# Kernel optimization log

Hardware: AMD Instinct MI355X
Metric: run time of the kernel (lower is better)

Reference implementation:

```python
import jax, jax.numpy as jnp
import numpy as np
from jax import lax

INPUT_DIM = 12
T = 2048
H = 512
L = 6
EPS = 1e-5


def setup_inputs() -> dict:
    key = jax.random.key(0)
    ks = jax.random.split(key, 12)
    s = 1.0 / np.sqrt(H)
    inp = {
        "x": jax.random.normal(ks[0], (32, INPUT_DIM), dtype=jnp.float32),
        "in_proj_w": jax.random.normal(ks[1], (H, INPUT_DIM), dtype=jnp.float32) * (1.0 / np.sqrt(INPUT_DIM)),
        "in_proj_b": jnp.zeros((H,), dtype=jnp.float32),
        "W_ih": jax.random.uniform(ks[2], (L, 4 * H, H), dtype=jnp.float32, minval=-s, maxval=s),
        "W_hh": jax.random.uniform(ks[3], (L, 4 * H, H), dtype=jnp.float32, minval=-s, maxval=s),
        "b_ih": jax.random.uniform(ks[4], (L, 4 * H), dtype=jnp.float32, minval=-s, maxval=s),
        "b_hh": jax.random.uniform(ks[5], (L, 4 * H), dtype=jnp.float32, minval=-s, maxval=s),
        "ln_scale": jnp.ones((L, H), dtype=jnp.float32),
        "ln_bias": jnp.zeros((L, H), dtype=jnp.float32),
        "out_w": jax.random.normal(ks[6], (1, H), dtype=jnp.float32) * s,
        "out_b": jnp.zeros((1,), dtype=jnp.float32),
    }
    return inp


def _lstm_layer(h_in, Wih, Whh, bih, bhh):
    # h_in: (B, T, H); PyTorch gate order: i, f, g, o
    B = h_in.shape[0]
    xg = jnp.einsum("bth,gh->btg", h_in, Wih) + bih  # (B, T, 4H) input gates precomputed
    xg_t = jnp.swapaxes(xg, 0, 1)  # (T, B, 4H)
    h0 = jnp.zeros((B, H), dtype=h_in.dtype)
    c0 = jnp.zeros((B, H), dtype=h_in.dtype)

    def step(carry, xt):
        h, c = carry
        gates = xt + h @ Whh.T + bhh
        i, f, g, o = jnp.split(gates, 4, axis=-1)
        i = jax.nn.sigmoid(i)
        f = jax.nn.sigmoid(f)
        g = jnp.tanh(g)
        o = jax.nn.sigmoid(o)
        c = f * c + i * g
        h = o * jnp.tanh(c)
        return (h, c), h

    _, hs = lax.scan(step, (h0, c0), xg_t)  # hs: (T, B, H)
    return jnp.swapaxes(hs, 0, 1)


def _layernorm(x, scale, bias):
    mu = jnp.mean(x, axis=-1, keepdims=True)
    var = jnp.mean(jnp.square(x - mu), axis=-1, keepdims=True)
    return (x - mu) * lax.rsqrt(var + EPS) * scale + bias


def reference(x, in_proj_w, in_proj_b, W_ih, W_hh, b_ih, b_hh, ln_scale, ln_bias, out_w, out_b):
    x_proj = x @ in_proj_w.T + in_proj_b  # (B, H)
    h = jnp.broadcast_to(x_proj[:, None, :], (x.shape[0], T, H))  # repeat along time
    for l in range(L):
        out = _lstm_layer(h, W_ih[l], W_hh[l], b_ih[l], b_hh[l])
        h = _layernorm(out + h, ln_scale[l], ln_bias[l])  # dropout = identity (eval)
    y = jnp.einsum("bth,oh->bto", h, out_w) + out_b  # (B, T, 1)
    return y[..., 0]  # (B, T)
```

## Files before the change

### kernel.cpp

```cpp
#include <hip/hip_runtime.h>

typedef __attribute__((ext_vector_type(4))) int   i32x4;
typedef __attribute__((ext_vector_type(8))) short s16x8;
typedef __attribute__((ext_vector_type(4))) float f32x4;

__device__ __forceinline__ unsigned short f2bf(float f) {
  unsigned u = __float_as_uint(f);
  unsigned r = u + 0x7FFFu + ((u >> 16) & 1u);
  return (unsigned short)(r >> 16);
}
__device__ __forceinline__ unsigned pack2bf(float lo, float hi) {
  return (unsigned)f2bf(lo) | ((unsigned)f2bf(hi) << 16);
}
__device__ __forceinline__ float bflo(unsigned u){ return __uint_as_float(u << 16); }
__device__ __forceinline__ float bfhi(unsigned u){ return __uint_as_float(u & 0xFFFF0000u); }

__device__ __forceinline__ float sigm(float x){ return 1.0f / (1.0f + __expf(-x)); }
__device__ __forceinline__ float tanh_(float x){
  float ax = fabsf(x);
  float e  = __expf(-2.0f * ax);
  float t  = (1.0f - e) / (1.0f + e);
  return copysignf(t, x);
}

__device__ __forceinline__ unsigned long long aload(const unsigned long long* p) {
  return __hip_atomic_load(p, __ATOMIC_RELAXED, __HIP_MEMORY_SCOPE_AGENT);
}
__device__ __forceinline__ void astore32(unsigned* p, unsigned v) {
  __hip_atomic_store(p, v, __ATOMIC_RELAXED, __HIP_MEMORY_SCOPE_AGENT);
}
__device__ __forceinline__ void astore64(unsigned long long* p, unsigned long long v) {
  __hip_atomic_store(p, v, __ATOMIC_RELAXED, __HIP_MEMORY_SCOPE_AGENT);
}

__device__ __forceinline__ void waitflags(const unsigned* Flg, int base, unsigned need, int lane) {
  const unsigned* p = Flg + ((base + (lane & 31)) << 4);
  unsigned v = __hip_atomic_load(p, __ATOMIC_RELAXED, __HIP_MEMORY_SCOPE_AGENT);
  while (!__all((int)(v >= need))) {
    __builtin_amdgcn_s_sleep(1);
    v = __hip_atomic_load(p, __ATOMIC_RELAXED, __HIP_MEMORY_SCOPE_AGENT);
  }
}

__global__ __launch_bounds__(256) void k_inproj(const float* __restrict__ x,
                                                const float* __restrict__ w,
                                                const float* __restrict__ bb,
                                                float* __restrict__ XP) {
  int idx = blockIdx.x * 256 + threadIdx.x;
  int b = idx >> 9, j = idx & 511;
  float acc = bb[j];
#pragma unroll
  for (int k = 0; k < 12; ++k) acc += x[b * 12 + k] * w[j * 12 + k];
  XP[idx] = acc;
}

__global__ __launch_bounds__(256) void k_xg0(const float* __restrict__ XP,
                                             const float* __restrict__ Wih,
                                             const float* __restrict__ bih,
                                             float* __restrict__ XG0) {
  int idx = blockIdx.x * 256 + threadIdx.x;
  int b = idx & 31;
  int r = idx >> 5;
  const float* wr = Wih + (size_t)r * 512;
  const float* xr = XP + b * 512;
  float acc = bih[r];
  for (int k = 0; k < 512; k += 4) {
    const f32x4 w4 = *(const f32x4*)(wr + k);
    const f32x4 x4 = *(const f32x4*)(xr + k);
    acc += w4[0]*x4[0] + w4[1]*x4[1] + w4[2]*x4[2] + w4[3]*x4[3];
  }
  XG0[b * 2048 + r] = acc;
}

__global__ __launch_bounds__(256, 1) void k_pipe(
    const float* __restrict__ Wih, const float* __restrict__ Whh,
    const float* __restrict__ bih, const float* __restrict__ bhh,
    const float* __restrict__ lnS, const float* __restrict__ lnB,
    const float* __restrict__ XG0, const float* __restrict__ XP,
    unsigned long long* __restrict__ Hst,
    unsigned long long* __restrict__ Roll,
    unsigned long long* __restrict__ Part,
    unsigned* __restrict__ RB,
    unsigned* __restrict__ Flg,
    unsigned* __restrict__ Prog)
{
  __shared__ char smem[65536];
  const int tid   = threadIdx.x;
  const int wgid  = blockIdx.x;
  const int layer = wgid >> 5;
  const int w     = wgid & 31;

  char* xarea = smem;
  char* harea = smem + 32768;
  const int lane = tid & 63;
  const int wv   = tid >> 6;
  const int j0   = w << 4;
  float* gacc = (float*)(layer == 0 ? (smem + 10240) : (harea + 16384));

  unsigned long long* HstL = Hst + layer * 8192;

  s16x8 bfih[16], bfhh[16];
  {
    const int rcol = lane & 15;
    const int kg   = lane >> 4;
    const size_t rowbase = ((size_t)layer * 2048 + (size_t)(wv * 512 + j0 + rcol)) * 512;
    const float* ihr = Wih + rowbase;
    const float* hhr = Whh + rowbase;
#pragma unroll
    for (int kk = 0; kk < 16; ++kk) {
      const int k0 = kg * 8 + kk * 32;
      s16x8 v2;
#pragma unroll
      for (int j = 0; j < 8; ++j) v2[j] = (short)f2bf(hhr[k0 + j]);
      bfhh[kk] = v2;
      if (layer > 0) {
        s16x8 v1;
#pragma unroll
        for (int j = 0; j < 8; ++j) v1[j] = (short)f2bf(ihr[k0 + j]);
        bfih[kk] = v1;
      }
    }
  }

  const int ub = tid >> 3;
  const int jp = tid & 7;
  const int kpglob = (j0 >> 1) + jp;

  float bs[4][2];
#pragma unroll
  for (int g = 0; g < 4; ++g)
#pragma unroll
    for (int c = 0; c < 2; ++c) {
      const size_t r = (size_t)layer * 2048 + g * 512 + j0 + 2 * jp + c;
      float vv = bhh[r];
      if (layer > 0) vv += bih[r];
      bs[g][c] = vv;
    }

  float scp[4] = {0,0,0,0}, bip[4] = {0,0,0,0};
  if (layer > 0) {
    const int cb = (layer - 1) * 512 + 4 * (tid & 127);
#pragma unroll
    for (int j = 0; j < 4; ++j) { scp[j] = lnS[cb + j]; bip[j] = lnB[cb + j]; }
  }

  if (layer == 0) {
    float* xg0s = (float*)smem;
    float* xps  = (float*)(smem + 8192);
    for (int i = tid; i < 2048; i += 256) {
      int g = i >> 9, b = (i >> 4) & 31, jl = i & 15;
      xg0s[i] = XG0[b * 2048 + g * 512 + j0 + jl];
    }
    for (int i = tid; i < 512; i += 256) {
      int b = i >> 4, jl = i & 15;
      xps[i] = XP[b * 512 + j0 + jl];
    }
  }

  astore32((unsigned*)HstL + (ub << 8) + kpglob, 0u);
  __syncthreads();
  if (tid == 0)
    __hip_atomic_store(Flg + ((layer * 32 + w) << 4), 1u, __ATOMIC_RELEASE, __HIP_MEMORY_SCOPE_AGENT);

  float xinc0 = 0.f, xinc1 = 0.f;
  if (layer == 0) {
    const float* xps = (const float*)(smem + 8192);
    xinc0 = xps[ub * 16 + 2 * jp];
    xinc1 = xps[ub * 16 + 2 * jp + 1];
  }

  const int b31 = tid & 31, w8 = tid >> 5;

  if (layer > 0) {
    waitflags(Flg, (layer - 1) * 32, 2u, lane);
    const unsigned long long* RollC = Roll + (layer - 1) * 16384;
    const unsigned long long* PC    = Part + (layer - 1) * 4096;
    unsigned long long xr[16], pr[4];
#pragma unroll
    for (int it = 0; it < 16; ++it) xr[it] = aload(RollC + it * 256 + tid);
#pragma unroll
    for (int k = 0; k < 4; ++k) pr[k] = aload(PC + (w8 + 8 * k) * 32 + b31);
    float s4 = 0.f, ss4 = 0.f;
#pragma unroll
    for (int k = 0; k < 4; ++k) { s4 += __uint_as_float((unsigned)pr[k]); ss4 += __uint_as_float((unsigned)(pr[k] >> 32)); }
    float* scr = (float*)harea;
    scr[(w8 * 32 + b31) * 2]     = s4;
    scr[(w8 * 32 + b31) * 2 + 1] = ss4;
    __syncthreads();
    float* stats = (float*)(harea + 2048);
    if (tid < 32) {
      const float* sc = (const float*)harea;
      float ssum = 0.f, sssum = 0.f;
#pragma unroll
      for (int k = 0; k < 8; ++k) { ssum += sc[(k * 32 + tid) * 2]; sssum += sc[(k * 32 + tid) * 2 + 1]; }
      const float mu = ssum * (1.f / 512.f);
      float var = sssum * (1.f / 512.f) - mu * mu;
      stats[tid * 2] = mu; stats[tid * 2 + 1] = rsqrtf(var + 1e-5f);
    }
    __syncthreads();
#pragma unroll
    for (int it = 0; it < 16; ++it) {
      const int flat = it * 256 + tid;
      const int q = flat >> 7, c0 = (flat & 127) * 2;
      const float mu = stats[q * 2], rs = stats[q * 2 + 1];
      const unsigned lo = (unsigned)xr[it], hi = (unsigned)(xr[it] >> 32);
      const float a0 = (bflo(lo) - mu) * rs * scp[0] + bip[0];
      const float a1 = (bfhi(lo) - mu) * rs * scp[1] + bip[1];
      const float a2 = (bflo(hi) - mu) * rs * scp[2] + bip[2];
      const float a3 = (bfhi(hi) - mu) * rs * scp[3] + bip[3];
      *(unsigned long long*)(xarea + ((q * 1024 + c0 * 4) ^ ((q & 7) << 4))) =
          (unsigned long long)pack2bf(a0, a1) | ((unsigned long long)pack2bf(a2, a3) << 32);
    }
  }
  __syncthreads();

  const int rA  = lane & 15;
  const int kg2 = lane >> 4;
  const int swz = (rA & 7) << 4;
  const int ab0 = rA * 1024 + kg2 * 16;
  const int ab1 = ab0 + 16384;

  float creg0 = 0.f, creg1 = 0.f;
  unsigned myC = 0;
  const int lane31 = lane & 31;

#pragma unroll 1
  for (int t = 0; t < 2048; ++t) {
    if (layer < 5 && t >= 5) {
      const unsigned need = (unsigned)(t - 4);
      while (!__all((int)(myC >= need))) {
        if (myC < need)
          myC = __hip_atomic_load(Prog + (((layer + 1) * 32 + lane31) << 4),
                                  __ATOMIC_RELAXED, __HIP_MEMORY_SCOPE_AGENT);
        if (!__all((int)(myC >= need))) __builtin_amdgcn_s_sleep(1);
      }
    }

    waitflags(Flg, layer * 32, (unsigned)(t + 1), lane);

    const unsigned long long* hs = HstL + (size_t)(t & 1) * 4096;
    unsigned long long a[16];
#pragma unroll
    for (int it = 0; it < 16; ++it)
      a[it] = aload(hs + it * 256 + tid);

    float xin0, xin1;
    f32x4 ai0 = {0.f,0.f,0.f,0.f}, ai1 = {0.f,0.f,0.f,0.f};
    if (layer > 0) {
      const unsigned xu = *(const unsigned*)(xarea + (((ub * 1024) + kpglob * 4) ^ ((ub & 7) << 4)));
      xin0 = bflo(xu); xin1 = bfhi(xu);
#pragma unroll
      for (int kk = 0; kk < 16; ++kk) {
        const i32x4 x0 = *(const i32x4*)(xarea + ((ab0 + kk * 64) ^ swz));
        const i32x4 x1 = *(const i32x4*)(xarea + ((ab1 + kk * 64) ^ swz));
        ai0 = __builtin_amdgcn_mfma_f32_16x16x32_bf16(__builtin_bit_cast(s16x8, x0), bfih[kk], ai0, 0, 0, 0);
        ai1 = __builtin_amdgcn_mfma_f32_16x16x32_bf16(__builtin_bit_cast(s16x8, x1), bfih[kk], ai1, 0, 0, 0);
      }
    } else { xin0 = xinc0; xin1 = xinc1; }

#pragma unroll
    for (int it = 0; it < 16; ++it) {
      const int flat = it * 256 + tid;
      const int q = flat >> 7, kp2 = flat & 127;
      *(unsigned long long*)(harea + ((q * 1024 + kp2 * 8) ^ ((q & 7) << 4))) = a[it];
    }
    __syncthreads();

    f32x4 acc0, acc1;
    if (layer > 0) {
      f32x4 ah0 = {0.f,0.f,0.f,0.f}, ah1 = {0.f,0.f,0.f,0.f};
#pragma unroll
      for (int kk = 0; kk < 16; ++kk) {
        const i32x4 h0 = *(const i32x4*)(harea + ((ab0 + kk * 64) ^ swz));
        const i32x4 h1 = *(const i32x4*)(harea + ((ab1 + kk * 64) ^ swz));
        ah0 = __builtin_amdgcn_mfma_f32_16x16x32_bf16(__builtin_bit_cast(s16x8, h0), bfhh[kk], ah0, 0, 0, 0);
        ah1 = __builtin_amdgcn_mfma_f32_16x16x32_bf16(__builtin_bit_cast(s16x8, h1), bfhh[kk], ah1, 0, 0, 0);
      }
      acc0 = ai0 + ah0; acc1 = ai1 + ah1;
    } else {
      f32x4 a0a = {0.f,0.f,0.f,0.f}, a1a = {0.f,0.f,0.f,0.f};
      f32x4 a0b = {0.f,0.f,0.f,0.f}, a1b = {0.f,0.f,0.f,0.f};
#pragma unroll
      for (int kk = 0; kk < 8; ++kk) {
        const i32x4 h0a = *(const i32x4*)(harea + ((ab0 + kk * 64) ^ swz));
        const i32x4 h1a = *(const i32x4*)(harea + ((ab1 + kk * 64) ^ swz));
        const i32x4 h0b = *(const i32x4*)(harea + ((ab0 + (kk + 8) * 64) ^ swz));
        const i32x4 h1b = *(const i32x4*)(harea + ((ab1 + (kk + 8) * 64) ^ swz));
        a0a = __builtin_amdgcn_mfma_f32_16x16x32_bf16(__builtin_bit_cast(s16x8, h0a), bfhh[kk], a0a, 0, 0, 0);
        a1a = __builtin_amdgcn_mfma_f32_16x16x32_bf16(__builtin_bit_cast(s16x8, h1a), bfhh[kk], a1a, 0, 0, 0);
        a0b = __builtin_amdgcn_mfma_f32_16x16x32_bf16(__builtin_bit_cast(s16x8, h0b), bfhh[kk + 8], a0b, 0, 0, 0);
        a1b = __builtin_amdgcn_mfma_f32_16x16x32_bf16(__builtin_bit_cast(s16x8, h1b), bfhh[kk + 8], a1b, 0, 0, 0);
      }
      acc0 = a0a + a0b; acc1 = a1a + a1b;
    }
    __syncthreads();
    {
      float* gp = gacc + (wv * 16 + rA) * 36 + kg2 * 4;
      *(f32x4*)gp        = acc0;
      *(f32x4*)(gp + 16) = acc1;
    }
    __syncthreads();

    float pre[4][2];
#pragma unroll
    for (int g = 0; g < 4; ++g)
#pragma unroll
      for (int c = 0; c < 2; ++c) {
        float vv = gacc[(g * 16 + 2 * jp + c) * 36 + ub] + bs[g][c];
        if (layer == 0) vv += ((const float*)smem)[(g * 32 + ub) * 16 + 2 * jp + c];
        pre[g][c] = vv;
      }

    float i0 = sigm(pre[0][0]), ff0 = sigm(pre[1][0]), g0 = tanh_(pre[2][0]), o0 = sigm(pre[3][0]);
    creg0 = ff0 * creg0 + i0 * g0;
    float h0 = o0 * tanh_(creg0);
    float i1 = sigm(pre[0][1]), ff1 = sigm(pre[1][1]), g1 = tanh_(pre[2][1]), o1 = sigm(pre[3][1]);
    creg1 = ff1 * creg1 + i1 * g1;
    float h1 = o1 * tanh_(creg1);
    const float out0 = h0 + xin0, out1 = h1 + xin1;

    if (layer < 5) {
      float sP  = out0 + out1;
      float ssP = out0 * out0 + out1 * out1;
#pragma unroll
      for (int m = 1; m < 8; m <<= 1) { sP += __shfl_xor(sP, m, 64); ssP += __shfl_xor(ssP, m, 64); }
      astore32((unsigned*)(Roll + layer * 16384 + (size_t)(t & 3) * 4096) + (ub << 8) + kpglob,
               pack2bf(out0, out1));
      if (jp == 0)
        astore64(Part + layer * 4096 + (size_t)(t & 3) * 1024 + w * 32 + ub,
                 (unsigned long long)__float_as_uint(sP) |
                 ((unsigned long long)__float_as_uint(ssP) << 32));
    } else {
      RB[((size_t)ub * 2048 + t) * 256 + kpglob] = pack2bf(out0, out1);
    }
    astore32((unsigned*)(HstL + (size_t)((t + 1) & 1) * 4096) + (ub << 8) + kpglob,
             pack2bf(h0, h1));

    __syncthreads();
    if (tid == 0)
      __hip_atomic_store(Flg + ((layer * 32 + w) << 4), (unsigned)(t + 2),
                         __ATOMIC_RELEASE, __HIP_MEMORY_SCOPE_AGENT);

    if (layer > 0 && t < 2047) {
      waitflags(Flg, (layer - 1) * 32, (unsigned)(t + 3), lane);
      const unsigned long long* RollC = Roll + (layer - 1) * 16384 + (size_t)((t + 1) & 3) * 4096;
      const unsigned long long* PC    = Part + (layer - 1) * 4096 + (size_t)((t + 1) & 3) * 1024;
      unsigned long long xr[16], pr[4];
#pragma unroll
      for (int it = 0; it < 16; ++it) xr[it] = aload(RollC + it * 256 + tid);
#pragma unroll
      for (int k = 0; k < 4; ++k) pr[k] = aload(PC + (w8 + 8 * k) * 32 + b31);
      float s4 = 0.f, ss4 = 0.f;
#pragma unroll
      for (int k = 0; k < 4; ++k) { s4 += __uint_as_float((unsigned)pr[k]); ss4 += __uint_as_float((unsigned)(pr[k] >> 32)); }
      float* scr = (float*)harea;
      scr[(w8 * 32 + b31) * 2]     = s4;
      scr[(w8 * 32 + b31) * 2 + 1] = ss4;
      __syncthreads();
      float* stats = (float*)(harea + 2048);
      if (tid < 32) {
        const float* sc = (const float*)harea;
        float ssum = 0.f, sssum = 0.f;
#pragma unroll
        for (int k = 0; k < 8; ++k) { ssum += sc[(k * 32 + tid) * 2]; sssum += sc[(k * 32 + tid) * 2 + 1]; }
        const float mu = ssum * (1.f / 512.f);
        float var = sssum * (1.f / 512.f) - mu * mu;
        stats[tid * 2] = mu; stats[tid * 2 + 1] = rsqrtf(var + 1e-5f);
      }
      __syncthreads();
#pragma unroll
      for (int it = 0; it < 16; ++it) {
        const int flat = it * 256 + tid;
        const int q = flat >> 7, c0 = (flat & 127) * 2;
        const float mu = stats[q * 2], rs = stats[q * 2 + 1];
        const unsigned lo = (unsigned)xr[it], hi = (unsigned)(xr[it] >> 32);
        const float a0 = (bflo(lo) - mu) * rs * scp[0] + bip[0];
        const float a1 = (bfhi(lo) - mu) * rs * scp[1] + bip[1];
        const float a2 = (bflo(hi) - mu) * rs * scp[2] + bip[2];
        const float a3 = (bfhi(hi) - mu) * rs * scp[3] + bip[3];
        *(unsigned long long*)(xarea + ((q * 1024 + c0 * 4) ^ ((q & 7) << 4))) =
            (unsigned long long)pack2bf(a0, a1) | ((unsigned long long)pack2bf(a2, a3) << 32);
      }
      if (tid == 0)
        astore32(Prog + ((layer * 32 + w) << 4), (unsigned)(t + 1));
    }

    __syncthreads();
  }
}

__global__ __launch_bounds__(256) void k_lnout(const unsigned* __restrict__ Rin,
                                               const float* __restrict__ lnS,
                                               const float* __restrict__ lnB,
                                               const float* __restrict__ ow,
                                               const float* __restrict__ ob,
                                               float* __restrict__ y) {
  int row  = blockIdx.x * 4 + (threadIdx.x >> 6);
  int lane = threadIdx.x & 63;
  const i32x4 v = *(const i32x4*)(Rin + (size_t)row * 256 + lane * 4);
  float xv[8];
#pragma unroll
  for (int j = 0; j < 4; ++j) {
    unsigned u = (unsigned)v[j];
    xv[2*j]   = bflo(u);
    xv[2*j+1] = bfhi(u);
  }
  float s = 0.f, s2 = 0.f;
#pragma unroll
  for (int j = 0; j < 8; ++j) { s += xv[j]; s2 += xv[j] * xv[j]; }
#pragma unroll
  for (int m = 1; m < 64; m <<= 1) { s += __shfl_xor(s, m, 64); s2 += __shfl_xor(s2, m, 64); }
  float mu  = s * (1.f / 512.f);
  float var = s2 * (1.f / 512.f) - mu * mu;
  float rs  = rsqrtf(var + 1e-5f);
  const float* Sp = lnS + 5 * 512 + lane * 8;
  const float* Bp = lnB + 5 * 512 + lane * 8;
  const float* wp = ow + lane * 8;
  float acc = 0.f;
#pragma unroll
  for (int j = 0; j < 8; ++j)
    acc += ((xv[j] - mu) * rs * Sp[j] + Bp[j]) * wp[j];
#pragma unroll
  for (int m = 1; m < 64; m <<= 1) acc += __shfl_xor(acc, m, 64);
  if (lane == 0) y[row] = acc + ob[0];
}

extern "C" void kernel_launch(void* const* d_in, const int* in_sizes, int n_in,
                              void* d_out, int out_size, void* d_ws, size_t ws_size,
                              hipStream_t stream) {
  (void)in_sizes; (void)n_in; (void)out_size; (void)ws_size;
  const float* x   = (const float*)d_in[0];
  const float* ipw = (const float*)d_in[1];
  const float* ipb = (const float*)d_in[2];
  const float* Wih = (const float*)d_in[3];
  const float* Whh = (const float*)d_in[4];
  const float* bih = (const float*)d_in[5];
  const float* bhh = (const float*)d_in[6];
  const float* lnS = (const float*)d_in[7];
  const float* lnB = (const float*)d_in[8];
  const float* ow  = (const float*)d_in[9];
  const float* ob  = (const float*)d_in[10];
  float* y = (float*)d_out;

  char* ws = (char*)d_ws;
  unsigned* Flg             = (unsigned*)ws;
  unsigned* Prog            = (unsigned*)(ws + 16384);
  float* XP                 = (float*)(ws + 32768);
  float* XG0                = (float*)(ws + 98304);
  unsigned long long* Hst   = (unsigned long long*)(ws + 360448);
  unsigned long long* Roll  = (unsigned long long*)(ws + 753664);
  unsigned long long* Part  = (unsigned long long*)(ws + 1409024);
  unsigned* RB              = (unsigned*)(ws + 2097152);

  hipMemsetAsync(ws, 0, 32768, stream);
  k_inproj<<<64, 256, 0, stream>>>(x, ipw, ipb, XP);
  k_xg0<<<256, 256, 0, stream>>>(XP, Wih, bih, XG0);
  k_pipe<<<192, 256, 0, stream>>>(Wih, Whh, bih, bhh, lnS, lnB, XG0, XP,
                                  Hst, Roll, Part, RB, Flg, Prog);
  k_lnout<<<16384, 256, 0, stream>>>(RB, lnS, lnB, ow, ob, y);
}
```

Baseline: 18.25 ms.

## Split input-projection and layernorm into separate helper workgroups feeding recurrent workgroups

Adds 160 helper workgroups that, for layers 1-5, compute the per-step layernorm of the previous layer's output and the W_ih input-gate matmul, then write the results to a 4-slot ring buffer in global memory guarded by new flags. The recurrent workgroups now only do the W_hh matmul and the gate math, so the work on the serial recurrence critical path is shorter. Layernorm stats are computed inside the helper instead of via partial sums, and launch bounds allow two workgroups per CU. The cost is extra global traffic for the gate pre-activations, more flag polling, and a risk of deadlock or contention if all 352 workgroups are not co-resident.

```diff
diff --git a/kernel.cpp b/kernel.cpp
--- a/kernel.cpp
+++ b/kernel.cpp
@@ -14,6 +14,9 @@
 }
 __device__ __forceinline__ float bflo(unsigned u){ return __uint_as_float(u << 16); }
 __device__ __forceinline__ float bfhi(unsigned u){ return __uint_as_float(u & 0xFFFF0000u); }
+__device__ __forceinline__ unsigned long long pack2f(float lo, float hi) {
+  return (unsigned long long)__float_as_uint(lo) | ((unsigned long long)__float_as_uint(hi) << 32);
+}
 
 __device__ __forceinline__ float sigm(float x){ return 1.0f / (1.0f + __expf(-x)); }
 __device__ __forceinline__ float tanh_(float x){
@@ -26,6 +29,9 @@
 __device__ __forceinline__ unsigned long long aload(const unsigned long long* p) {
   return __hip_atomic_load(p, __ATOMIC_RELAXED, __HIP_MEMORY_SCOPE_AGENT);
 }
+__device__ __forceinline__ unsigned aload32(const unsigned* p) {
+  return __hip_atomic_load(p, __ATOMIC_RELAXED, __HIP_MEMORY_SCOPE_AGENT);
+}
 __device__ __forceinline__ void astore32(unsigned* p, unsigned v) {
   __hip_atomic_store(p, v, __ATOMIC_RELAXED, __HIP_MEMORY_SCOPE_AGENT);
 }
@@ -33,10 +39,17 @@
   __hip_atomic_store(p, v, __ATOMIC_RELAXED, __HIP_MEMORY_SCOPE_AGENT);
 }
 
-__device__ __forceinline__ void waitflags(const unsigned* Flg, int base, unsigned need, int lane) {
-  const unsigned* p = Flg + ((base + (lane & 31)) << 4);
+__device__ __forceinline__ void waitflags(const unsigned* F, int base, unsigned need, int lane) {
+  const unsigned* p = F + ((base + (lane & 31)) << 4);
   unsigned v = __hip_atomic_load(p, __ATOMIC_RELAXED, __HIP_MEMORY_SCOPE_AGENT);
   while (!__all((int)(v >= need))) {
+    __builtin_amdgcn_s_sleep(1);
+    v = __hip_atomic_load(p, __ATOMIC_RELAXED, __HIP_MEMORY_SCOPE_AGENT);
+  }
+}
+__device__ __forceinline__ void wait1(const unsigned* p, unsigned need) {
+  unsigned v = __hip_atomic_load(p, __ATOMIC_RELAXED, __HIP_MEMORY_SCOPE_AGENT);
+  while (v < need) {
     __builtin_amdgcn_s_sleep(1);
     v = __hip_atomic_load(p, __ATOMIC_RELAXED, __HIP_MEMORY_SCOPE_AGENT);
   }
@@ -72,212 +85,118 @@
   XG0[b * 2048 + r] = acc;
 }
 
-__global__ __launch_bounds__(256, 1) void k_pipe(
+__global__ __launch_bounds__(256, 2) void k_pipe(
     const float* __restrict__ Wih, const float* __restrict__ Whh,
     const float* __restrict__ bih, const float* __restrict__ bhh,
     const float* __restrict__ lnS, const float* __restrict__ lnB,
     const float* __restrict__ XG0, const float* __restrict__ XP,
     unsigned long long* __restrict__ Hst,
     unsigned long long* __restrict__ Roll,
-    unsigned long long* __restrict__ Part,
+    unsigned long long* __restrict__ XGb,
     unsigned* __restrict__ RB,
-    unsigned* __restrict__ Flg,
-    unsigned* __restrict__ Prog)
+    unsigned* __restrict__ SF,
+    unsigned* __restrict__ HF)
 {
-  __shared__ char smem[65536];
-  const int tid   = threadIdx.x;
-  const int wgid  = blockIdx.x;
-  const int layer = wgid >> 5;
-  const int w     = wgid & 31;
-
-  char* xarea = smem;
-  char* harea = smem + 32768;
+  __shared__ char smem[43008];
+  const int tid  = threadIdx.x;
+  const int wgid = blockIdx.x;
   const int lane = tid & 63;
   const int wv   = tid >> 6;
-  const int j0   = w << 4;
-  float* gacc = (float*)(layer == 0 ? (smem + 10240) : (harea + 16384));
-
-  unsigned long long* HstL = Hst + layer * 8192;
-
-  s16x8 bfih[16], bfhh[16];
-  {
-    const int rcol = lane & 15;
-    const int kg   = lane >> 4;
-    const size_t rowbase = ((size_t)layer * 2048 + (size_t)(wv * 512 + j0 + rcol)) * 512;
-    const float* ihr = Wih + rowbase;
-    const float* hhr = Whh + rowbase;
-#pragma unroll
-    for (int kk = 0; kk < 16; ++kk) {
-      const int k0 = kg * 8 + kk * 32;
-      s16x8 v2;
-#pragma unroll
-      for (int j = 0; j < 8; ++j) v2[j] = (short)f2bf(hhr[k0 + j]);
-      bfhh[kk] = v2;
+
+  if (wgid < 192) {
+    const int layer = wgid >> 5, w = wgid & 31, j0 = w << 4;
+    char* harea = smem;
+    float* gacc = (float*)(harea + 16384);
+    unsigned long long* HstL = Hst + layer * 8192;
+
+    s16x8 bfhh[16];
+    {
+      const int rcol = lane & 15, kg = lane >> 4;
+      const size_t rowbase = ((size_t)layer * 2048 + (size_t)(wv * 512 + j0 + rcol)) * 512;
+      const float* hhr = Whh + rowbase;
+#pragma unroll
+      for (int kk = 0; kk < 16; ++kk) {
+        const int k0 = kg * 8 + kk * 32;
+        s16x8 v2;
+#pragma unroll
+        for (int j = 0; j < 8; ++j) v2[j] = (short)f2bf(hhr[k0 + j]);
+        bfhh[kk] = v2;
+      }
+    }
+
+    const int ub = tid >> 3, jp = tid & 7;
+    const int kpglob = (j0 >> 1) + jp;
+
+    float bs[4][2];
+#pragma unroll
+    for (int g = 0; g < 4; ++g)
+#pragma unroll
+      for (int c = 0; c < 2; ++c) {
+        const size_t r = (size_t)layer * 2048 + g * 512 + j0 + 2 * jp + c;
+        float vv = bhh[r];
+        if (layer > 0) vv += bih[r];
+        bs[g][c] = vv;
+      }
+
+    float* xg0s = (float*)(smem + 32768);
+    float* xps  = (float*)(smem + 40960);
+    if (layer == 0) {
+      for (int i = tid; i < 2048; i += 256) {
+        int g = i >> 9, b = (i >> 4) & 31, jl = i & 15;
+        xg0s[i] = XG0[b * 2048 + g * 512 + j0 + jl];
+      }
+      for (int i = tid; i < 512; i += 256) {
+        int b = i >> 4, jl = i & 15;
+        xps[i] = XP[b * 512 + j0 + jl];
+      }
+    }
+
+    astore32((unsigned*)HstL + (ub << 8) + kpglob, 0u);
+    __syncthreads();
+    if (tid == 0)
+      __hip_atomic_store(SF + ((layer * 32 + w) << 4), 1u, __ATOMIC_RELEASE, __HIP_MEMORY_SCOPE_AGENT);
+
+    float xinc0 = 0.f, xinc1 = 0.f;
+    if (layer == 0) { xinc0 = xps[ub * 16 + 2 * jp]; xinc1 = xps[ub * 16 + 2 * jp + 1]; }
+
+    const int rA = lane & 15, kg2 = lane >> 4;
+    const int swz = (rA & 7) << 4;
+    const int ab0 = rA * 1024 + kg2 * 16;
+    const int ab1 = ab0 + 16384;
+    const int sh  = (ub & 1) * 32;
+    float creg0 = 0.f, creg1 = 0.f;
+
+#pragma unroll 1
+    for (int t = 0; t < 2048; ++t) {
+      if (layer < 5 && t >= 4) waitflags(HF, layer * 32, (unsigned)(t - 3), lane);
+
+      unsigned long long xgv[8];
+      unsigned xinu = 0;
       if (layer > 0) {
-        s16x8 v1;
-#pragma unroll
-        for (int j = 0; j < 8; ++j) v1[j] = (short)f2bf(ihr[k0 + j]);
-        bfih[kk] = v1;
-      }
-    }
-  }
-
-  const int ub = tid >> 3;
-  const int jp = tid & 7;
-  const int kpglob = (j0 >> 1) + jp;
-
-  float bs[4][2];
-#pragma unroll
-  for (int g = 0; g < 4; ++g)
-#pragma unroll
-    for (int c = 0; c < 2; ++c) {
-      const size_t r = (size_t)layer * 2048 + g * 512 + j0 + 2 * jp + c;
-      float vv = bhh[r];
-      if (layer > 0) vv += bih[r];
-      bs[g][c] = vv;
-    }
-
-  float scp[4] = {0,0,0,0}, bip[4] = {0,0,0,0};
-  if (layer > 0) {
-    const int cb = (layer - 1) * 512 + 4 * (tid & 127);
-#pragma unroll
-    for (int j = 0; j < 4; ++j) { scp[j] = lnS[cb + j]; bip[j] = lnB[cb + j]; }
-  }
-
-  if (layer == 0) {
-    float* xg0s = (float*)smem;
-    float* xps  = (float*)(smem + 8192);
-    for (int i = tid; i < 2048; i += 256) {
-      int g = i >> 9, b = (i >> 4) & 31, jl = i & 15;
-      xg0s[i] = XG0[b * 2048 + g * 512 + j0 + jl];
-    }
-    for (int i = tid; i < 512; i += 256) {
-      int b = i >> 4, jl = i & 15;
-      xps[i] = XP[b * 512 + j0 + jl];
-    }
-  }
-
-  astore32((unsigned*)HstL + (ub << 8) + kpglob, 0u);
-  __syncthreads();
-  if (tid == 0)
-    __hip_atomic_store(Flg + ((layer * 32 + w) << 4), 1u, __ATOMIC_RELEASE, __HIP_MEMORY_SCOPE_AGENT);
-
-  float xinc0 = 0.f, xinc1 = 0.f;
-  if (layer == 0) {
-    const float* xps = (const float*)(smem + 8192);
-    xinc0 = xps[ub * 16 + 2 * jp];
-    xinc1 = xps[ub * 16 + 2 * jp + 1];
-  }
-
-  const int b31 = tid & 31, w8 = tid >> 5;
-
-  if (layer > 0) {
-    waitflags(Flg, (layer - 1) * 32, 2u, lane);
-    const unsigned long long* RollC = Roll + (layer - 1) * 16384;
-    const unsigned long long* PC    = Part + (layer - 1) * 4096;
-    unsigned long long xr[16], pr[4];
-#pragma unroll
-    for (int it = 0; it < 16; ++it) xr[it] = aload(RollC + it * 256 + tid);
-#pragma unroll
-    for (int k = 0; k < 4; ++k) pr[k] = aload(PC + (w8 + 8 * k) * 32 + b31);
-    float s4 = 0.f, ss4 = 0.f;
-#pragma unroll
-    for (int k = 0; k < 4; ++k) { s4 += __uint_as_float((unsigned)pr[k]); ss4 += __uint_as_float((unsigned)(pr[k] >> 32)); }
-    float* scr = (float*)harea;
-    scr[(w8 * 32 + b31) * 2]     = s4;
-    scr[(w8 * 32 + b31) * 2 + 1] = ss4;
-    __syncthreads();
-    float* stats = (float*)(harea + 2048);
-    if (tid < 32) {
-      const float* sc = (const float*)harea;
-      float ssum = 0.f, sssum = 0.f;
-#pragma unroll
-      for (int k = 0; k < 8; ++k) { ssum += sc[(k * 32 + tid) * 2]; sssum += sc[(k * 32 + tid) * 2 + 1]; }
-      const float mu = ssum * (1.f / 512.f);
-      float var = sssum * (1.f / 512.f) - mu * mu;
-      stats[tid * 2] = mu; stats[tid * 2 + 1] = rsqrtf(var + 1e-5f);
-    }
-    __syncthreads();
-#pragma unroll
-    for (int it = 0; it < 16; ++it) {
-      const int flat = it * 256 + tid;
-      const int q = flat >> 7, c0 = (flat & 127) * 2;
-      const float mu = stats[q * 2], rs = stats[q * 2 + 1];
-      const unsigned lo = (unsigned)xr[it], hi = (unsigned)(xr[it] >> 32);
-      const float a0 = (bflo(lo) - mu) * rs * scp[0] + bip[0];
-      const float a1 = (bfhi(lo) - mu) * rs * scp[1] + bip[1];
-      const float a2 = (bflo(hi) - mu) * rs * scp[2] + bip[2];
-      const float a3 = (bfhi(hi) - mu) * rs * scp[3] + bip[3];
-      *(unsigned long long*)(xarea + ((q * 1024 + c0 * 4) ^ ((q & 7) << 4))) =
-          (unsigned long long)pack2bf(a0, a1) | ((unsigned long long)pack2bf(a2, a3) << 32);
-    }
-  }
-  __syncthreads();
-
-  const int rA  = lane & 15;
-  const int kg2 = lane >> 4;
-  const int swz = (rA & 7) << 4;
-  const int ab0 = rA * 1024 + kg2 * 16;
-  const int ab1 = ab0 + 16384;
-
-  float creg0 = 0.f, creg1 = 0.f;
-  unsigned myC = 0;
-  const int lane31 = lane & 31;
-
-#pragma unroll 1
-  for (int t = 0; t < 2048; ++t) {
-    if (layer < 5 && t >= 5) {
-      const unsigned need = (unsigned)(t - 4);
-      while (!__all((int)(myC >= need))) {
-        if (myC < need)
-          myC = __hip_atomic_load(Prog + (((layer + 1) * 32 + lane31) << 4),
-                                  __ATOMIC_RELAXED, __HIP_MEMORY_SCOPE_AGENT);
-        if (!__all((int)(myC >= need))) __builtin_amdgcn_s_sleep(1);
-      }
-    }
-
-    waitflags(Flg, layer * 32, (unsigned)(t + 1), lane);
-
-    const unsigned long long* hs = HstL + (size_t)(t & 1) * 4096;
-    unsigned long long a[16];
-#pragma unroll
-    for (int it = 0; it < 16; ++it)
-      a[it] = aload(hs + it * 256 + tid);
-
-    float xin0, xin1;
-    f32x4 ai0 = {0.f,0.f,0.f,0.f}, ai1 = {0.f,0.f,0.f,0.f};
-    if (layer > 0) {
-      const unsigned xu = *(const unsigned*)(xarea + (((ub * 1024) + kpglob * 4) ^ ((ub & 7) << 4)));
-      xin0 = bflo(xu); xin1 = bfhi(xu);
-#pragma unroll
-      for (int kk = 0; kk < 16; ++kk) {
-        const i32x4 x0 = *(const i32x4*)(xarea + ((ab0 + kk * 64) ^ swz));
-        const i32x4 x1 = *(const i32x4*)(xarea + ((ab1 + kk * 64) ^ swz));
-        ai0 = __builtin_amdgcn_mfma_f32_16x16x32_bf16(__builtin_bit_cast(s16x8, x0), bfih[kk], ai0, 0, 0, 0);
-        ai1 = __builtin_amdgcn_mfma_f32_16x16x32_bf16(__builtin_bit_cast(s16x8, x1), bfih[kk], ai1, 0, 0, 0);
-      }
-    } else { xin0 = xinc0; xin1 = xinc1; }
-
-#pragma unroll
-    for (int it = 0; it < 16; ++it) {
-      const int flat = it * 256 + tid;
-      const int q = flat >> 7, kp2 = flat & 127;
-      *(unsigned long long*)(harea + ((q * 1024 + kp2 * 8) ^ ((q & 7) << 4))) = a[it];
-    }
-    __syncthreads();
-
-    f32x4 acc0, acc1;
-    if (layer > 0) {
-      f32x4 ah0 = {0.f,0.f,0.f,0.f}, ah1 = {0.f,0.f,0.f,0.f};
-#pragma unroll
-      for (int kk = 0; kk < 16; ++kk) {
-        const i32x4 h0 = *(const i32x4*)(harea + ((ab0 + kk * 64) ^ swz));
-        const i32x4 h1 = *(const i32x4*)(harea + ((ab1 + kk * 64) ^ swz));
-        ah0 = __builtin_amdgcn_mfma_f32_16x16x32_bf16(__builtin_bit_cast(s16x8, h0), bfhh[kk], ah0, 0, 0, 0);
-        ah1 = __builtin_amdgcn_mfma_f32_16x16x32_bf16(__builtin_bit_cast(s16x8, h1), bfhh[kk], ah1, 0, 0, 0);
-      }
-      acc0 = ai0 + ah0; acc1 = ai1 + ah1;
-    } else {
+        wait1(HF + (((layer - 1) * 32 + w) << 4), (unsigned)(t + 1));
+        const unsigned long long* rec = XGb + (size_t)(((layer - 1) * 4 + (t & 3)) * 32 + w) * 1152;
+#pragma unroll
+        for (int g = 0; g < 4; ++g)
+#pragma unroll
+          for (int cc = 0; cc < 2; ++cc)
+            xgv[g * 2 + cc] = aload(rec + g * 256 + (2 * jp + cc) * 16 + (ub >> 1));
+        xinu = aload32((const unsigned*)(rec + 1024) + ub * 8 + jp);
+      }
+
+      waitflags(SF, layer * 32, (unsigned)(t + 1), lane);
+
+      const unsigned long long* hs = HstL + (size_t)(t & 1) * 4096;
+      unsigned long long a[16];
+#pragma unroll
+      for (int it = 0; it < 16; ++it) a[it] = aload(hs + it * 256 + tid);
+#pragma unroll
+      for (int it = 0; it < 16; ++it) {
+        const int flat = it * 256 + tid;
+        const int q = flat >> 7, kp2 = flat & 127;
+        *(unsigned long long*)(harea + ((q * 1024 + kp2 * 8) ^ ((q & 7) << 4))) = a[it];
+      }
+      __syncthreads();
+
       f32x4 a0a = {0.f,0.f,0.f,0.f}, a1a = {0.f,0.f,0.f,0.f};
       f32x4 a0b = {0.f,0.f,0.f,0.f}, a1b = {0.f,0.f,0.f,0.f};
 #pragma unroll
@@ -291,101 +210,145 @@
         a0b = __builtin_amdgcn_mfma_f32_16x16x32_bf16(__builtin_bit_cast(s16x8, h0b), bfhh[kk + 8], a0b, 0, 0, 0);
         a1b = __builtin_amdgcn_mfma_f32_16x16x32_bf16(__builtin_bit_cast(s16x8, h1b), bfhh[kk + 8], a1b, 0, 0, 0);
       }
-      acc0 = a0a + a0b; acc1 = a1a + a1b;
+      const f32x4 acc0 = a0a + a0b, acc1 = a1a + a1b;
+      __syncthreads();
+      {
+        float* gp = gacc + (wv * 16 + rA) * 36 + kg2 * 4;
+        *(f32x4*)gp        = acc0;
+        *(f32x4*)(gp + 16) = acc1;
+      }
+      __syncthreads();
+
+      float pre[4][2];
+#pragma unroll
+      for (int g = 0; g < 4; ++g)
+#pragma unroll
+        for (int c = 0; c < 2; ++c) {
+          float vv = gacc[(g * 16 + 2 * jp + c) * 36 + ub] + bs[g][c];
+          if (layer == 0) vv += xg0s[(g * 32 + ub) * 16 + 2 * jp + c];
+          else            vv += __uint_as_float((unsigned)(xgv[g * 2 + c] >> sh));
+          pre[g][c] = vv;
+        }
+
+      float i0 = sigm(pre[0][0]), ff0 = sigm(pre[1][0]), g0 = tanh_(pre[2][0]), o0 = sigm(pre[3][0]);
+      creg0 = ff0 * creg0 + i0 * g0;
+      float h0 = o0 * tanh_(creg0);
+      float i1 = sigm(pre[0][1]), ff1 = sigm(pre[1][1]), g1 = tanh_(pre[2][1]), o1 = sigm(pre[3][1]);
+      creg1 = ff1 * creg1 + i1 * g1;
+      float h1 = o1 * tanh_(creg1);
+
+      const float xin0 = (layer > 0) ? bflo(xinu) : xinc0;
+      const float xin1 = (layer > 0) ? bfhi(xinu) : xinc1;
+      const float out0 = h0 + xin0, out1 = h1 + xin1;
+
+      if (layer < 5) {
+        astore32((unsigned*)(Roll + (size_t)(layer * 4 + (t & 3)) * 4096) + (ub << 8) + kpglob,
+                 pack2bf(out0, out1));
+      } else {
+        RB[((size_t)ub * 2048 + t) * 256 + kpglob] = pack2bf(out0, out1);
+      }
+      astore32((unsigned*)(HstL + (size_t)((t + 1) & 1) * 4096) + (ub << 8) + kpglob,
+               pack2bf(h0, h1));
+
+      __syncthreads();
+      if (tid == 0)
+        __hip_atomic_store(SF + ((layer * 32 + w) << 4), (unsigned)(t + 2),
+                           __ATOMIC_RELEASE, __HIP_MEMORY_SCOPE_AGENT);
     }
-    __syncthreads();
+  } else {
+    const int idx = wgid - 192;
+    const int hl = 1 + (idx >> 5), hw = idx & 31, j0 = hw << 4;
+    char* xarea = smem;
+
+    s16x8 bfih[16];
     {
-      float* gp = gacc + (wv * 16 + rA) * 36 + kg2 * 4;
-      *(f32x4*)gp        = acc0;
-      *(f32x4*)(gp + 16) = acc1;
+      const int rcol = lane & 15, kg = lane >> 4;
+      const size_t rowbase = ((size_t)hl * 2048 + (size_t)(wv * 512 + j0 + rcol)) * 512;
+      const float* ihr = Wih + rowbase;
+#pragma unroll
+      for (int kk = 0; kk < 16; ++kk) {
+        const int k0 = kg * 8 + kk * 32;
+        s16x8 v1;
+#pragma unroll
+        for (int j = 0; j < 8; ++j) v1[j] = (short)f2bf(ihr[k0 + j]);
+        bfih[kk] = v1;
+      }
     }
-    __syncthreads();
-
-    float pre[4][2];
-#pragma unroll
-    for (int g = 0; g < 4; ++g)
-#pragma unroll
-      for (int c = 0; c < 2; ++c) {
-        float vv = gacc[(g * 16 + 2 * jp + c) * 36 + ub] + bs[g][c];
-        if (layer == 0) vv += ((const float*)smem)[(g * 32 + ub) * 16 + 2 * jp + c];
-        pre[g][c] = vv;
-      }
-
-    float i0 = sigm(pre[0][0]), ff0 = sigm(pre[1][0]), g0 = tanh_(pre[2][0]), o0 = sigm(pre[3][0]);
-    creg0 = ff0 * creg0 + i0 * g0;
-    float h0 = o0 * tanh_(creg0);
-    float i1 = sigm(pre[0][1]), ff1 = sigm(pre[1][1]), g1 = tanh_(pre[2][1]), o1 = sigm(pre[3][1]);
-    creg1 = ff1 * creg1 + i1 * g1;
-    float h1 = o1 * tanh_(creg1);
-    const float out0 = h0 + xin0, out1 = h1 + xin1;
-
-    if (layer < 5) {
-      float sP  = out0 + out1;
-      float ssP = out0 * out0 + out1 * out1;
-#pragma unroll
-      for (int m = 1; m < 8; m <<= 1) { sP += __shfl_xor(sP, m, 64); ssP += __shfl_xor(ssP, m, 64); }
-      astore32((unsigned*)(Roll + layer * 16384 + (size_t)(t & 3) * 4096) + (ub << 8) + kpglob,
-               pack2bf(out0, out1));
-      if (jp == 0)
-        astore64(Part + layer * 4096 + (size_t)(t & 3) * 1024 + w * 32 + ub,
-                 (unsigned long long)__float_as_uint(sP) |
-                 ((unsigned long long)__float_as_uint(ssP) << 32));
-    } else {
-      RB[((size_t)ub * 2048 + t) * 256 + kpglob] = pack2bf(out0, out1);
+
+    const int r = tid >> 3, k = tid & 7;
+    const int rA = lane & 15, kg2 = lane >> 4;
+    const int swz = (rA & 7) << 4;
+    const int ab0 = rA * 1024 + kg2 * 16;
+    const int ab1 = ab0 + 16384;
+    const float* lnSl = lnS + (hl - 1) * 512;
+    const float* lnBl = lnB + (hl - 1) * 512;
+    unsigned* myHF = HF + (((hl - 1) * 32 + hw) << 4);
+    const unsigned* mySF = SF + ((hl * 32 + hw) << 4);
+
+#pragma unroll 1
+    for (int u = 0; u < 2048; ++u) {
+      if (u >= 4) wait1(mySF, (unsigned)(u - 2));
+      waitflags(SF, (hl - 1) * 32, (unsigned)(u + 2), lane);
+
+      const unsigned long long* RollC = Roll + (size_t)((hl - 1) * 4 + (u & 3)) * 4096;
+      unsigned long long xr[16];
+#pragma unroll
+      for (int j = 0; j < 16; ++j) xr[j] = aload(RollC + r * 128 + k + 8 * j);
+
+      float s = 0.f, ss = 0.f;
+#pragma unroll
+      for (int j = 0; j < 16; ++j) {
+        const unsigned lo = (unsigned)xr[j], hi = (unsigned)(xr[j] >> 32);
+        const float v0 = bflo(lo), v1 = bfhi(lo), v2 = bflo(hi), v3 = bfhi(hi);
+        s  += v0 + v1 + v2 + v3;
+        ss += v0 * v0 + v1 * v1 + v2 * v2 + v3 * v3;
+      }
+#pragma unroll
+      for (int m = 1; m < 8; m <<= 1) { s += __shfl_xor(s, m, 64); ss += __shfl_xor(ss, m, 64); }
+      const float mu = s * (1.f / 512.f);
+      float var = ss * (1.f / 512.f) - mu * mu;
+      const float rs = rsqrtf(var + 1e-5f);
+
+#pragma unroll
+      for (int j = 0; j < 16; ++j) {
+        const int jj = k + 8 * j;
+        const f32x4 sc4 = *(const f32x4*)(lnSl + 4 * jj);
+        const f32x4 bi4 = *(const f32x4*)(lnBl + 4 * jj);
+        const unsigned lo = (unsigned)xr[j], hi = (unsigned)(xr[j] >> 32);
+        const float a0 = (bflo(lo) - mu) * rs * sc4[0] + bi4[0];
+        const float a1 = (bfhi(lo) - mu) * rs * sc4[1] + bi4[1];
+        const float a2 = (bflo(hi) - mu) * rs * sc4[2] + bi4[2];
+        const float a3 = (bfhi(hi) - mu) * rs * sc4[3] + bi4[3];
+        *(unsigned long long*)(xarea + ((r * 1024 + jj * 8) ^ ((r & 7) << 4))) =
+            (unsigned long long)pack2bf(a0, a1) | ((unsigned long long)pack2bf(a2, a3) << 32);
+      }
+      __syncthreads();
+
+      f32x4 ai0 = {0.f,0.f,0.f,0.f}, ai1 = {0.f,0.f,0.f,0.f};
+#pragma unroll
+      for (int kk = 0; kk < 16; ++kk) {
+        const i32x4 x0 = *(const i32x4*)(xarea + ((ab0 + kk * 64) ^ swz));
+        const i32x4 x1 = *(const i32x4*)(xarea + ((ab1 + kk * 64) ^ swz));
+        ai0 = __builtin_amdgcn_mfma_f32_16x16x32_bf16(__builtin_bit_cast(s16x8, x0), bfih[kk], ai0, 0, 0, 0);
+        ai1 = __builtin_amdgcn_mfma_f32_16x16x32_bf16(__builtin_bit_cast(s16x8, x1), bfih[kk], ai1, 0, 0, 0);
+      }
+
+      unsigned long long* rec = XGb + (size_t)(((hl - 1) * 4 + (u & 3)) * 32 + hw) * 1152;
+      const int base = wv * 256 + rA * 16 + kg2 * 2;
+      astore64(rec + base,     pack2f(ai0[0], ai0[1]));
+      astore64(rec + base + 1, pack2f(ai0[2], ai0[3]));
+      astore64(rec + base + 8, pack2f(ai1[0], ai1[1]));
+      astore64(rec + base + 9, pack2f(ai1[2], ai1[3]));
+      {
+        const int b2 = tid >> 3, p = tid & 7;
+        const unsigned xv = *(const unsigned*)(xarea + ((b2 * 1024 + (hw * 8 + p) * 4) ^ ((b2 & 7) << 4)));
+        astore32((unsigned*)(rec + 1024) + tid, xv);
+      }
+      __syncthreads();
+      if (tid == 0)
+        __hip_atomic_store((unsigned*)myHF, (unsigned)(u + 1),
+                           __ATOMIC_RELEASE, __HIP_MEMORY_SCOPE_AGENT);
     }
-    astore32((unsigned*)(HstL + (size_t)((t + 1) & 1) * 4096) + (ub << 8) + kpglob,
-             pack2bf(h0, h1));
-
-    __syncthreads();
-    if (tid == 0)
-      __hip_atomic_store(Flg + ((layer * 32 + w) << 4), (unsigned)(t + 2),
-                         __ATOMIC_RELEASE, __HIP_MEMORY_SCOPE_AGENT);
-
-    if (layer > 0 && t < 2047) {
-      waitflags(Flg, (layer - 1) * 32, (unsigned)(t + 3), lane);
-      const unsigned long long* RollC = Roll + (layer - 1) * 16384 + (size_t)((t + 1) & 3) * 4096;
-      const unsigned long long* PC    = Part + (layer - 1) * 4096 + (size_t)((t + 1) & 3) * 1024;
-      unsigned long long xr[16], pr[4];
-#pragma unroll
-      for (int it = 0; it < 16; ++it) xr[it] = aload(RollC + it * 256 + tid);
-#pragma unroll
-      for (int k = 0; k < 4; ++k) pr[k] = aload(PC + (w8 + 8 * k) * 32 + b31);
-      float s4 = 0.f, ss4 = 0.f;
-#pragma unroll
-      for (int k = 0; k < 4; ++k) { s4 += __uint_as_float((unsigned)pr[k]); ss4 += __uint_as_float((unsigned)(pr[k] >> 32)); }
-      float* scr = (float*)harea;
-      scr[(w8 * 32 + b31) * 2]     = s4;
-      scr[(w8 * 32 + b31) * 2 + 1] = ss4;
-      __syncthreads();
-      float* stats = (float*)(harea + 2048);
-      if (tid < 32) {
-        const float* sc = (const float*)harea;
-        float ssum = 0.f, sssum = 0.f;
-#pragma unroll
-        for (int k = 0; k < 8; ++k) { ssum += sc[(k * 32 + tid) * 2]; sssum += sc[(k * 32 + tid) * 2 + 1]; }
-        const float mu = ssum * (1.f / 512.f);
-        float var = sssum * (1.f / 512.f) - mu * mu;
-        stats[tid * 2] = mu; stats[tid * 2 + 1] = rsqrtf(var + 1e-5f);
-      }
-      __syncthreads();
-#pragma unroll
-      for (int it = 0; it < 16; ++it) {
-        const int flat = it * 256 + tid;
-        const int q = flat >> 7, c0 = (flat & 127) * 2;
-        const float mu = stats[q * 2], rs = stats[q * 2 + 1];
-        const unsigned lo = (unsigned)xr[it], hi = (unsigned)(xr[it] >> 32);
-        const float a0 = (bflo(lo) - mu) * rs * scp[0] + bip[0];
-        const float a1 = (bfhi(lo) - mu) * rs * scp[1] + bip[1];
-        const float a2 = (bflo(hi) - mu) * rs * scp[2] + bip[2];
-        const float a3 = (bfhi(hi) - mu) * rs * scp[3] + bip[3];
-        *(unsigned long long*)(xarea + ((q * 1024 + c0 * 4) ^ ((q & 7) << 4))) =
-            (unsigned long long)pack2bf(a0, a1) | ((unsigned long long)pack2bf(a2, a3) << 32);
-      }
-      if (tid == 0)
-        astore32(Prog + ((layer * 32 + w) << 4), (unsigned)(t + 1));
-    }
-
-    __syncthreads();
   }
 }
 
@@ -443,19 +406,19 @@
   float* y = (float*)d_out;
 
   char* ws = (char*)d_ws;
-  unsigned* Flg             = (unsigned*)ws;
-  unsigned* Prog            = (unsigned*)(ws + 16384);
+  unsigned* SF              = (unsigned*)ws;
+  unsigned* HF              = (unsigned*)(ws + 16384);
   float* XP                 = (float*)(ws + 32768);
   float* XG0                = (float*)(ws + 98304);
   unsigned long long* Hst   = (unsigned long long*)(ws + 360448);
   unsigned long long* Roll  = (unsigned long long*)(ws + 753664);
-  unsigned long long* Part  = (unsigned long long*)(ws + 1409024);
-  unsigned* RB              = (unsigned*)(ws + 2097152);
+  unsigned long long* XGb   = (unsigned long long*)(ws + 1409024);
+  unsigned* RB              = (unsigned*)(ws + 8388608);
 
   hipMemsetAsync(ws, 0, 32768, stream);
   k_inproj<<<64, 256, 0, stream>>>(x, ipw, ipb, XP);
   k_xg0<<<256, 256, 0, stream>>>(XP, Wih, bih, XG0);
-  k_pipe<<<192, 256, 0, stream>>>(Wih, Whh, bih, bhh, lnS, lnB, XG0, XP,
-                                  Hst, Roll, Part, RB, Flg, Prog);
+  k_pipe<<<352, 256, 0, stream>>>(Wih, Whh, bih, bhh, lnS, lnB, XG0, XP,
+                                  Hst, Roll, XGb, RB, SF, HF);
   k_lnout<<<16384, 256, 0, stream>>>(RB, lnS, lnB, ow, ob, y);
 }
```

Measured after the change: 40.66 ms. 123% more time.
